# Performance work log

Measured on AMD Instinct MI355X. Metric: run time of the kernel, lower is better.

The kernel has to match this reference:

```python
import jax, jax.numpy as jnp
from jax import lax
import numpy as np

B = 1048576       # batched program states
L = 64            # hidden width of LinearNNComplex
STEPS = 19        # While test: state[5] < var(19), step counter +1 per iter


def setup_inputs() -> dict:
    key = jax.random.key(0)
    ks = jax.random.split(key, 7)
    x = jax.random.normal(ks[0], (B, 6), dtype=jnp.float32)
    x = x.at[:, 5].set(0.0)  # step counter starts at 0 so the While runs 19 iters
    # LinearNNComplex params: Linear(2,L) -> ReLU -> Linear(L,L) -> ReLU -> Linear(L,3) -> Sigmoid
    s1 = 1.0 / np.sqrt(2.0)
    s2 = 1.0 / np.sqrt(float(L))
    W1 = jax.random.normal(ks[1], (2, L), dtype=jnp.float32) * s1
    b1 = jax.random.normal(ks[2], (L,), dtype=jnp.float32) * s1
    W2 = jax.random.normal(ks[3], (L, L), dtype=jnp.float32) * s2
    b2 = jax.random.normal(ks[4], (L,), dtype=jnp.float32) * s2
    W3 = jax.random.normal(ks[5], (L, 3), dtype=jnp.float32) * s2
    b3 = jax.random.normal(ks[6], (3,), dtype=jnp.float32) * s2
    return {"x": x, "W1": W1, "b1": b1, "W2": W2, "b2": b2, "W3": W3, "b3": b3}


def reference(x, W1, b1, W2, b2, W3, b3):
    """Batched Program interpreter.

    State columns: [0]=position, [1]=forward counter, [2:5]=branch probs,
    [5]=step counter. Each iteration:
      state[2:5] = sigmoid-MLP(state[0:2])            (assign_branch_probability)
      argmax over cols 2,3,4 picks branch:            (argmax_p)
        0 -> move_up    (col0 -= 1)
        1 -> move_right (col0 unchanged)
        2 -> move_down  (col0 += 1)
      state[1] += 1                                   (forward_update)
      state[5] += 1                                   (step_update)
    Runs STEPS=19 iterations (While: state[5] < 19).
    """
    def nn(z):  # z: [B, 2]
        h = jax.nn.relu(z @ W1 + b1)
        h = jax.nn.relu(h @ W2 + b2)
        return jax.nn.sigmoid(h @ W3 + b3)  # [B, 3]

    def body(state, _):
        p = nn(state[:, :2])                         # [B, 3]
        idx = jnp.argmax(p, axis=-1)                 # [B]
        delta = (idx - 1).astype(state.dtype)        # up=-1, right=0, down=+1
        new = jnp.concatenate(
            [
                (state[:, 0] + delta)[:, None],
                (state[:, 1] + 1.0)[:, None],
                p,
                (state[:, 5] + 1.0)[:, None],
            ],
            axis=-1,
        )
        return new, None

    final, _ = lax.scan(body, x, None, length=STEPS)
    return final  # [B, 6]
```

## Files before the change

kernel.cpp:

```cpp
#include <hip/hip_runtime.h>
#include <math.h>


#define NSTEPS 19

typedef _Float16 half8   __attribute__((ext_vector_type(8)));
typedef _Float16 half2v  __attribute__((ext_vector_type(2)));
typedef float    float2v __attribute__((ext_vector_type(2)));
typedef float    float4v __attribute__((ext_vector_type(4)));
typedef unsigned int uint2v __attribute__((ext_vector_type(2)));

__device__ __forceinline__ half2v pkrtz(float a, float b) {
    return __builtin_bit_cast(half2v, __builtin_amdgcn_cvt_pkrtz(a, b));
}
__device__ __forceinline__ float2v lo2(float4v v) {
    return __builtin_shufflevector(v, v, 0, 1);
}
__device__ __forceinline__ float2v hi2(float4v v) {
    return __builtin_shufflevector(v, v, 2, 3);
}

__device__ __forceinline__ float xsum48(float g) {
#if __has_builtin(__builtin_amdgcn_permlane16_swap) && \
    __has_builtin(__builtin_amdgcn_permlane32_swap)
    unsigned u = __builtin_bit_cast(unsigned, g);
    uint2v a = __builtin_amdgcn_permlane16_swap(u, u, false, false);
    g = __builtin_bit_cast(float, (unsigned)a[0]) +
        __builtin_bit_cast(float, (unsigned)a[1]);
    unsigned v = __builtin_bit_cast(unsigned, g);
    uint2v b = __builtin_amdgcn_permlane32_swap(v, v, false, false);
    return __builtin_bit_cast(float, (unsigned)b[0]) +
           __builtin_bit_cast(float, (unsigned)b[1]);
#else
    int r = __builtin_amdgcn_ds_swizzle(__builtin_bit_cast(int, g), 0x401F);
    g += __builtin_bit_cast(float, r);
    g += __shfl_xor(g, 32, 64);
    return g;
#endif
}

__global__ __launch_bounds__(256, 2)
void program_kernel(const float* __restrict__ x,
                    const float* __restrict__ W1,
                    const float* __restrict__ b1,
                    const float* __restrict__ W2,
                    const float* __restrict__ b2,
                    const float* __restrict__ W3,
                    const float* __restrict__ b3,
                    float* __restrict__ out,
                    int B) {
    const int tid    = threadIdx.x;
    const int lane   = tid & 63;
    const int wave   = tid >> 6;
    const int lanelo = lane & 15;
    const int q8     = lane >> 4;
    const int myRow  = blockIdx.x * 64 + wave * 16 + lanelo;
    const int rowLd  = myRow < B ? myRow : (B - 1);

    float2v w1a[8], w1b[8], b1v[8];
    #pragma unroll
    for (int kf = 0; kf < 2; ++kf) {
        const int k0 = kf * 32 + q8 * 8;
        const float2v* a = (const float2v*)(W1 + k0);
        const float2v* bb = (const float2v*)(W1 + 64 + k0);
        const float2v* bv = (const float2v*)(b1 + k0);
        #pragma unroll
        for (int i = 0; i < 4; ++i) {
            w1a[kf * 4 + i] = a[i];
            w1b[kf * 4 + i] = bb[i];
            b1v[kf * 4 + i] = bv[i];
        }
    }

    half8 Wh[2][4], Wl[2][4];
    #pragma unroll
    for (int kf = 0; kf < 2; ++kf) {
        #pragma unroll
        for (int t = 0; t < 4; ++t) {
            half8 bh, bl;
            #pragma unroll
            for (int j = 0; j < 8; ++j) {
                const float w =
                    W2[(kf * 32 + q8 * 8 + j) * 64 + t * 16 + lanelo];
                const _Float16 wh = (_Float16)w;
                const _Float16 wl = (_Float16)((w - (float)wh) * 4096.0f);
                bh[j] = wh;
                bl[j] = wl;
            }
            Wh[kf][t] = bh;
            Wl[kf][t] = bl;
        }
    }

    float4v b2f[4];
    #pragma unroll
    for (int t = 0; t < 4; ++t) {
        const int n = t * 16 + q8 * 4;
        b2f[t] = (float4v){b2[n], b2[n + 1], b2[n + 2], b2[n + 3]};
    }

    float2v d10[8], d20[8];
    #pragma unroll
    for (int p = 0; p < 8; ++p) {
        const int n0 = (p >> 1) * 16 + q8 * 4 + (p & 1) * 2;
        const float w00 = W3[n0 * 3 + 0],       w01 = W3[n0 * 3 + 1];
        const float w02 = W3[n0 * 3 + 2];
        const float w10 = W3[(n0 + 1) * 3 + 0], w11 = W3[(n0 + 1) * 3 + 1];
        const float w12 = W3[(n0 + 1) * 3 + 2];
        d10[p] = (float2v){w01 - w00, w11 - w10};
        d20[p] = (float2v){w02 - w00, w12 - w10};
    }
    const float b3v0 = b3[0];
    const float db10 = b3[1] - b3[0];
    const float db20 = b3[2] - b3[0];

    float pos, fwd, c5;
    {
        const float* xr = x + (size_t)rowLd * 6;
        pos = xr[0];
        fwd = xr[1];
        c5  = xr[5];
    }

    const float4v zf = {0.f, 0.f, 0.f, 0.f};
    const float2v z2 = {0.f, 0.f};
    const float2v kinv = {1.0f / 4096.0f, 1.0f / 4096.0f};
    float l0 = 0.f, l1 = 0.f, l2 = 0.f;

    #pragma unroll 1
    for (int step = 0; step < NSTEPS; ++step) {
        const float2v posp = {pos, pos}, fwdp = {fwd, fwd};
        half8 Hh[2], Hl[2];
        #pragma unroll
        for (int kf = 0; kf < 2; ++kf) {
            union { half8 v; half2v h2[4]; } uh, ul;
            #pragma unroll
            for (int p = 0; p < 4; ++p) {
                const int e = kf * 4 + p;
                float2v z = __builtin_elementwise_fma(fwdp, w1b[e], b1v[e]);
                z = __builtin_elementwise_fma(posp, w1a[e], z);
                const float2v hp = __builtin_elementwise_max(z, z2);
                uh.h2[p] = pkrtz(hp[0], hp[1]);
                const float r0 = fmaf((float)uh.h2[p][0], -1.0f, hp[0]);
                const float r1 = fmaf((float)uh.h2[p][1], -1.0f, hp[1]);
                const float2v rp = (float2v){r0, r1} * 4096.0f;
                ul.h2[p] = pkrtz(rp[0], rp[1]);
            }
            Hh[kf] = uh.v;
            Hl[kf] = ul.v;
        }

        float4v accA[4], accB1[4], accB2[4];
        #pragma unroll
        for (int t = 0; t < 4; ++t) {
            accB1[t] = __builtin_amdgcn_mfma_f32_16x16x32_f16(
                Wl[0][t], Hh[0], zf, 0, 0, 0);
            accB1[t] = __builtin_amdgcn_mfma_f32_16x16x32_f16(
                Wh[0][t], Hl[0], accB1[t], 0, 0, 0);
            accB2[t] = __builtin_amdgcn_mfma_f32_16x16x32_f16(
                Wl[1][t], Hh[1], zf, 0, 0, 0);
            accB2[t] = __builtin_amdgcn_mfma_f32_16x16x32_f16(
                Wh[1][t], Hl[1], accB2[t], 0, 0, 0);
            accA[t] = __builtin_amdgcn_mfma_f32_16x16x32_f16(
                Wh[0][t], Hh[0], b2f[t], 0, 0, 0);
            accA[t] = __builtin_amdgcn_mfma_f32_16x16x32_f16(
                Wh[1][t], Hh[1], accA[t], 0, 0, 0);
        }

        float2v s1x = z2, s1y = z2, s2x = z2, s2y = z2;
        #pragma unroll
        for (int t = 0; t < 4; ++t) {
            const float4v aB = accB1[t] + accB2[t];
            const float2v h0 = __builtin_elementwise_max(
                __builtin_elementwise_fma(lo2(aB), kinv, lo2(accA[t])), z2);
            const float2v h1 = __builtin_elementwise_max(
                __builtin_elementwise_fma(hi2(aB), kinv, hi2(accA[t])), z2);
            s1x = __builtin_elementwise_fma(h0, d10[2 * t], s1x);
            s1y = __builtin_elementwise_fma(h1, d10[2 * t + 1], s1y);
            s2x = __builtin_elementwise_fma(h0, d20[2 * t], s2x);
            s2y = __builtin_elementwise_fma(h1, d20[2 * t + 1], s2y);
        }
        const float2v s1 = s1x + s1y;
        const float2v s2 = s2x + s2y;
        float g10 = s1[0] + s1[1];
        float g20 = s2[0] + s2[1];
        g10 = xsum48(g10) + db10;
        g20 = xsum48(g20) + db20;

        if (step == NSTEPS - 1) {
            float2v s0x = z2, s0y = z2;
            #pragma unroll
            for (int t = 0; t < 4; ++t) {
                const float4v aB = accB1[t] + accB2[t];
                const float2v h0 = __builtin_elementwise_max(
                    __builtin_elementwise_fma(lo2(aB), kinv, lo2(accA[t])), z2);
                const float2v h1 = __builtin_elementwise_max(
                    __builtin_elementwise_fma(hi2(aB), kinv, hi2(accA[t])), z2);
                const int n0 = t * 16 + q8 * 4;
                const float2v w3a = {W3[n0 * 3],       W3[(n0 + 1) * 3]};
                const float2v w3b = {W3[(n0 + 2) * 3], W3[(n0 + 3) * 3]};
                s0x = __builtin_elementwise_fma(h0, w3a, s0x);
                s0y = __builtin_elementwise_fma(h1, w3b, s0y);
            }
            const float2v s0 = s0x + s0y;
            float t0 = s0[0] + s0[1];
            t0 = xsum48(t0);
            l0 = t0 + b3v0;
            l1 = l0 + g10;
            l2 = l0 + g20;
        }

        const float delta =
            (g20 > fmaxf(0.f, g10)) ? 1.0f : ((g10 > 0.f) ? 0.0f : -1.0f);
        pos += delta;
        fwd += 1.0f;
    }

    if (q8 == 0 && myRow < B) {
        const float p0 = 1.f / (1.f + __expf(-l0));
        const float p1 = 1.f / (1.f + __expf(-l1));
        const float p2 = 1.f / (1.f + __expf(-l2));
        float2* o = (float2*)(out + (size_t)myRow * 6);
        o[0] = make_float2(pos, fwd);
        o[1] = make_float2(p0, p1);
        o[2] = make_float2(p2, c5 + (float)NSTEPS);
    }
}

extern "C" void kernel_launch(void* const* d_in, const int* in_sizes, int n_in,
                              void* d_out, int out_size, void* d_ws, size_t ws_size,
                              hipStream_t stream) {
    const float* x  = (const float*)d_in[0];
    const float* W1 = (const float*)d_in[1];
    const float* b1 = (const float*)d_in[2];
    const float* W2 = (const float*)d_in[3];
    const float* b2 = (const float*)d_in[4];
    const float* W3 = (const float*)d_in[5];
    const float* b3 = (const float*)d_in[6];
    float* out = (float*)d_out;

    const int B = in_sizes[0] / 6;
    const int nBlocks = (B + 63) / 64;

    program_kernel<<<nBlocks, 256, 0, stream>>>(
        x, W1, b1, W2, b2, W3, b3, out, B);
}
```

Measured before the change: 662.8 us.

## Interleave layer-1 compute with MFMA chains and merge split accumulators

Restructures the per-step body so the second half of layer-1 conversion is computed while the first-half MFMAs run, and the epilogue ReLU/dot work is interleaved with the trailing MFMAs, using sched_barriers to pin the order. The two low-part accumulators are merged into one chain, removing a vector add per tile, and the hidden activations are kept for reuse in the final-step W3 dot instead of being recomputed. This lengthens MFMA dependency chains and fixes instruction order manually, which may limit the compiler's own scheduling.

```diff
diff --git a/kernel.cpp b/kernel.cpp
--- a/kernel.cpp
+++ b/kernel.cpp
@@ -127,85 +127,98 @@
     const float2v kinv = {1.0f / 4096.0f, 1.0f / 4096.0f};
     float l0 = 0.f, l1 = 0.f, l2 = 0.f;
 
+    #define L1HALF(KF, HH, HL)                                                \
+        {                                                                     \
+            union { half8 v; half2v h2[4]; } uh, ul;                          \
+            _Pragma("unroll")                                                 \
+            for (int p = 0; p < 4; ++p) {                                     \
+                const int e = (KF) * 4 + p;                                   \
+                float2v z = __builtin_elementwise_fma(fwdp, w1b[e], b1v[e]);  \
+                z = __builtin_elementwise_fma(posp, w1a[e], z);               \
+                const float2v hp = __builtin_elementwise_max(z, z2);          \
+                uh.h2[p] = pkrtz(hp[0], hp[1]);                               \
+                const float r0 = fmaf((float)uh.h2[p][0], -1.0f, hp[0]);      \
+                const float r1 = fmaf((float)uh.h2[p][1], -1.0f, hp[1]);      \
+                const float2v rp = (float2v){r0, r1} * 4096.0f;               \
+                ul.h2[p] = pkrtz(rp[0], rp[1]);                               \
+            }                                                                 \
+            HH = uh.v;                                                        \
+            HL = ul.v;                                                        \
+        }
+
+    #define TRIO0(T)                                                          \
+        accB[T] = __builtin_amdgcn_mfma_f32_16x16x32_f16(                     \
+            Wl[0][T], Hh0, zf, 0, 0, 0);                                      \
+        accB[T] = __builtin_amdgcn_mfma_f32_16x16x32_f16(                     \
+            Wh[0][T], Hl0, accB[T], 0, 0, 0);                                 \
+        accA[T] = __builtin_amdgcn_mfma_f32_16x16x32_f16(                     \
+            Wh[0][T], Hh0, b2f[T], 0, 0, 0);
+
+    #define TRIO1(T)                                                          \
+        accB[T] = __builtin_amdgcn_mfma_f32_16x16x32_f16(                     \
+            Wl[1][T], Hh1, accB[T], 0, 0, 0);                                 \
+        accB[T] = __builtin_amdgcn_mfma_f32_16x16x32_f16(                     \
+            Wh[1][T], Hl1, accB[T], 0, 0, 0);                                 \
+        accA[T] = __builtin_amdgcn_mfma_f32_16x16x32_f16(                     \
+            Wh[1][T], Hh1, accA[T], 0, 0, 0);
+
+    #define CMBDOT(T)                                                         \
+        h2p[2 * (T)] = __builtin_elementwise_max(                             \
+            __builtin_elementwise_fma(lo2(accB[T]), kinv, lo2(accA[T])), z2); \
+        h2p[2 * (T) + 1] = __builtin_elementwise_max(                         \
+            __builtin_elementwise_fma(hi2(accB[T]), kinv, hi2(accA[T])), z2); \
+        s1 = __builtin_elementwise_fma(h2p[2 * (T)], d10[2 * (T)], s1);       \
+        s1 = __builtin_elementwise_fma(h2p[2 * (T) + 1], d10[2 * (T) + 1],    \
+                                       s1);                                   \
+        s2 = __builtin_elementwise_fma(h2p[2 * (T)], d20[2 * (T)], s2);       \
+        s2 = __builtin_elementwise_fma(h2p[2 * (T) + 1], d20[2 * (T) + 1],    \
+                                       s2);
+
     #pragma unroll 1
     for (int step = 0; step < NSTEPS; ++step) {
         const float2v posp = {pos, pos}, fwdp = {fwd, fwd};
-        half8 Hh[2], Hl[2];
-        #pragma unroll
-        for (int kf = 0; kf < 2; ++kf) {
-            union { half8 v; half2v h2[4]; } uh, ul;
+        half8 Hh0, Hl0, Hh1, Hl1;
+        float4v accA[4], accB[4];
+        float2v h2p[8];
+        float2v s1 = z2, s2 = z2;
+
+        L1HALF(0, Hh0, Hl0);
+        __builtin_amdgcn_sched_barrier(0);
+
+        TRIO0(0);
+        L1HALF(1, Hh1, Hl1);
+        TRIO0(1);
+        TRIO0(2);
+        TRIO0(3);
+        __builtin_amdgcn_sched_barrier(0);
+
+        TRIO1(0);
+        TRIO1(1);
+        __builtin_amdgcn_sched_barrier(0);
+
+        TRIO1(2);
+        CMBDOT(0);
+        __builtin_amdgcn_sched_barrier(0);
+
+        TRIO1(3);
+        CMBDOT(1);
+        __builtin_amdgcn_sched_barrier(0);
+
+        CMBDOT(2);
+        CMBDOT(3);
+
+        float g10 = xsum48(s1[0] + s1[1]) + db10;
+        float g20 = xsum48(s2[0] + s2[1]) + db20;
+
+        if (step == NSTEPS - 1) {
+            float2v s0 = z2;
             #pragma unroll
-            for (int p = 0; p < 4; ++p) {
-                const int e = kf * 4 + p;
-                float2v z = __builtin_elementwise_fma(fwdp, w1b[e], b1v[e]);
-                z = __builtin_elementwise_fma(posp, w1a[e], z);
-                const float2v hp = __builtin_elementwise_max(z, z2);
-                uh.h2[p] = pkrtz(hp[0], hp[1]);
-                const float r0 = fmaf((float)uh.h2[p][0], -1.0f, hp[0]);
-                const float r1 = fmaf((float)uh.h2[p][1], -1.0f, hp[1]);
-                const float2v rp = (float2v){r0, r1} * 4096.0f;
-                ul.h2[p] = pkrtz(rp[0], rp[1]);
+            for (int p = 0; p < 8; ++p) {
+                const int n0 = (p >> 1) * 16 + q8 * 4 + (p & 1) * 2;
+                const float2v w30 = {W3[n0 * 3], W3[(n0 + 1) * 3]};
+                s0 = __builtin_elementwise_fma(h2p[p], w30, s0);
             }
-            Hh[kf] = uh.v;
-            Hl[kf] = ul.v;
-        }
-
-        float4v accA[4], accB1[4], accB2[4];
-        #pragma unroll
-        for (int t = 0; t < 4; ++t) {
-            accB1[t] = __builtin_amdgcn_mfma_f32_16x16x32_f16(
-                Wl[0][t], Hh[0], zf, 0, 0, 0);
-            accB1[t] = __builtin_amdgcn_mfma_f32_16x16x32_f16(
-                Wh[0][t], Hl[0], accB1[t], 0, 0, 0);
-            accB2[t] = __builtin_amdgcn_mfma_f32_16x16x32_f16(
-                Wl[1][t], Hh[1], zf, 0, 0, 0);
-            accB2[t] = __builtin_amdgcn_mfma_f32_16x16x32_f16(
-                Wh[1][t], Hl[1], accB2[t], 0, 0, 0);
-            accA[t] = __builtin_amdgcn_mfma_f32_16x16x32_f16(
-                Wh[0][t], Hh[0], b2f[t], 0, 0, 0);
-            accA[t] = __builtin_amdgcn_mfma_f32_16x16x32_f16(
-                Wh[1][t], Hh[1], accA[t], 0, 0, 0);
-        }
-
-        float2v s1x = z2, s1y = z2, s2x = z2, s2y = z2;
-        #pragma unroll
-        for (int t = 0; t < 4; ++t) {
-            const float4v aB = accB1[t] + accB2[t];
-            const float2v h0 = __builtin_elementwise_max(
-                __builtin_elementwise_fma(lo2(aB), kinv, lo2(accA[t])), z2);
-            const float2v h1 = __builtin_elementwise_max(
-                __builtin_elementwise_fma(hi2(aB), kinv, hi2(accA[t])), z2);
-            s1x = __builtin_elementwise_fma(h0, d10[2 * t], s1x);
-            s1y = __builtin_elementwise_fma(h1, d10[2 * t + 1], s1y);
-            s2x = __builtin_elementwise_fma(h0, d20[2 * t], s2x);
-            s2y = __builtin_elementwise_fma(h1, d20[2 * t + 1], s2y);
-        }
-        const float2v s1 = s1x + s1y;
-        const float2v s2 = s2x + s2y;
-        float g10 = s1[0] + s1[1];
-        float g20 = s2[0] + s2[1];
-        g10 = xsum48(g10) + db10;
-        g20 = xsum48(g20) + db20;
-
-        if (step == NSTEPS - 1) {
-            float2v s0x = z2, s0y = z2;
-            #pragma unroll
-            for (int t = 0; t < 4; ++t) {
-                const float4v aB = accB1[t] + accB2[t];
-                const float2v h0 = __builtin_elementwise_max(
-                    __builtin_elementwise_fma(lo2(aB), kinv, lo2(accA[t])), z2);
-                const float2v h1 = __builtin_elementwise_max(
-                    __builtin_elementwise_fma(hi2(aB), kinv, hi2(accA[t])), z2);
-                const int n0 = t * 16 + q8 * 4;
-                const float2v w3a = {W3[n0 * 3],       W3[(n0 + 1) * 3]};
-                const float2v w3b = {W3[(n0 + 2) * 3], W3[(n0 + 3) * 3]};
-                s0x = __builtin_elementwise_fma(h0, w3a, s0x);
-                s0y = __builtin_elementwise_fma(h1, w3b, s0y);
-            }
-            const float2v s0 = s0x + s0y;
-            float t0 = s0[0] + s0[1];
-            t0 = xsum48(t0);
-            l0 = t0 + b3v0;
+            l0 = xsum48(s0[0] + s0[1]) + b3v0;
             l1 = l0 + g10;
             l2 = l0 + g20;
         }
```

New measurement: 657.2 us. No clear change (-0.8%).
